# Performance work log

Hardware: AMD Instinct MI355X
Metric: run time of the kernel (lower is better)

The kernel has to match this reference:

```python
import jax, jax.numpy as jnp
import numpy as np

N_PER_TYPE = 32000
N = 3 * N_PER_TYPE          # 96000 nodes
E = N * 16                  # 1,536,000 edges
H, D = 4, 8                 # num_heads, out_dim per head; hidden = 32
IN_DIMS = [128, 64, 32]
NEG_SLOPE = 0.2


def setup_inputs() -> dict:
    key = jax.random.key(0)
    ks = jax.random.split(key, 16)
    inp = {}
    # per-type raw features
    inp['x0'] = jax.random.normal(ks[0], (N_PER_TYPE, IN_DIMS[0]), jnp.float32)
    inp['x1'] = jax.random.normal(ks[1], (N_PER_TYPE, IN_DIMS[1]), jnp.float32)
    inp['x2'] = jax.random.normal(ks[2], (N_PER_TYPE, IN_DIMS[2]), jnp.float32)
    # per-type linear params (fc_list), scaled like kaiming-ish init
    inp['W0'] = jax.random.normal(ks[3], (IN_DIMS[0], H * D), jnp.float32) / np.sqrt(IN_DIMS[0])
    inp['b0'] = jnp.zeros((H * D,), jnp.float32)
    inp['W1'] = jax.random.normal(ks[4], (IN_DIMS[1], H * D), jnp.float32) / np.sqrt(IN_DIMS[1])
    inp['b1'] = jnp.zeros((H * D,), jnp.float32)
    inp['W2'] = jax.random.normal(ks[5], (IN_DIMS[2], H * D), jnp.float32) / np.sqrt(IN_DIMS[2])
    inp['b2'] = jnp.zeros((H * D,), jnp.float32)
    # GAT attention vectors a_l, a_r per head
    inp['attn_l'] = jax.random.normal(ks[6], (H, D), jnp.float32) / np.sqrt(D)
    inp['attn_r'] = jax.random.normal(ks[7], (H, D), jnp.float32) / np.sqrt(D)
    # node types laid out in contiguous blocks -> fixed-size index sets
    inp['type_mask'] = jnp.repeat(jnp.arange(3, dtype=jnp.int32), N_PER_TYPE)
    inp['idx0'] = jnp.arange(0, N_PER_TYPE, dtype=jnp.int32)
    inp['idx1'] = jnp.arange(N_PER_TYPE, 2 * N_PER_TYPE, dtype=jnp.int32)
    inp['idx2'] = jnp.arange(2 * N_PER_TYPE, 3 * N_PER_TYPE, dtype=jnp.int32)
    # random edge list
    inp['src'] = jax.random.randint(ks[8], (E,), 0, N, jnp.int32)
    inp['dst'] = jax.random.randint(ks[9], (E,), 0, N, jnp.int32)
    return inp


def reference(x0, x1, x2, W0, b0, W1, b1, W2, b2, attn_l, attn_r,
              idx0, idx1, idx2, src, dst, type_mask):
    # ---- type-masked per-type linear embed scattered into dense buffer ----
    t = jnp.zeros((N, H * D), x0.dtype)
    t = t.at[idx0].set(x0 @ W0 + b0)
    t = t.at[idx1].set(x1 @ W1 + b1)
    t = t.at[idx2].set(x2 @ W2 + b2)
    # (feat_drop is identity in eval mode)
    h = t.reshape(N, H, D)
    # ---- multi-head GAT attention ----
    el = jnp.einsum('nhd,hd->nh', h, attn_l)   # [N,H]
    er = jnp.einsum('nhd,hd->nh', h, attn_r)   # [N,H]
    e = jax.nn.leaky_relu(el[src] + er[dst], NEG_SLOPE)  # [E,H]
    # segment softmax over incoming edges of each dst node
    m = jax.ops.segment_max(e, dst, num_segments=N)      # [N,H]
    m = jnp.where(jnp.isfinite(m), m, 0.0)               # guard isolated nodes
    ex = jnp.exp(e - m[dst])                             # [E,H]
    s = jax.ops.segment_sum(ex, dst, num_segments=N)     # [N,H]
    alpha = ex / (s[dst] + 1e-9)                         # [E,H]
    # message aggregation
    msg = alpha[:, :, None] * h[src]                     # [E,H,D]
    out = jax.ops.segment_sum(msg, dst, num_segments=N)  # [N,H,D]
    # concat heads + ELU (standard intermediate-layer GAT activation)
    return jax.nn.elu(out).reshape(N, H * D)
```

## Files before the change

kernel.cpp:

```cpp
#include <hip/hip_runtime.h>
#include <hip/hip_bf16.h>
#include <math.h>

#define N_PER_TYPE 32000
#define NN (3 * N_PER_TYPE)
#define EDGES (NN * 16)
#define NHEAD 4
#define HD 32
#define NEG 0.2f
#define BINS 256
#define NPB (NN / BINS)
#define TILES 512
#define TPE (EDGES / TILES)
#define SEG 32
#define MAXBIN 8192
#define EB 375
#define QCH ((TILES * SEG) / 1024)

typedef __attribute__((ext_vector_type(8))) short bf16x8;
typedef __attribute__((ext_vector_type(4))) float f32x4;

__device__ __forceinline__ unsigned packbf(float a, float b) {
    __hip_bfloat162 t = __float22bfloat162_rn(make_float2(a, b));
    return *reinterpret_cast<unsigned*>(&t);
}

__global__ __launch_bounds__(1024) void fused1_kernel(
    const float* __restrict__ x0, const float* __restrict__ x1, const float* __restrict__ x2,
    const float* __restrict__ W0, const float* __restrict__ b0,
    const float* __restrict__ W1, const float* __restrict__ b1,
    const float* __restrict__ W2, const float* __restrict__ b2,
    const float* __restrict__ attn_l, const float* __restrict__ attn_r,
    const int* __restrict__ src, const int* __restrict__ dst,
    __hip_bfloat16* __restrict__ h16, float* __restrict__ el, float* __restrict__ er,
    unsigned* __restrict__ rec2, int* __restrict__ cntT)
{
    __shared__ __align__(16) char smem[43008];
    int blk = blockIdx.x;
    int tid = threadIdx.x;

    if (blk < TILES) {
        int* hist = (int*)smem;
        int* pref = (int*)(smem + 1024);
        unsigned* sorted = (unsigned*)(smem + 2048);
        unsigned char* binof = (unsigned char*)(smem + 2048 + TPE * 4);
        int tile = blk;

        for (int i = tid; i < BINS; i += 1024) hist[i] = 0;
        __syncthreads();

        int e0 = tile * TPE;
        unsigned rv[3]; int rb[3], rk[3]; int ne = 0;
        for (int t = e0 + tid; t < e0 + TPE; t += 1024) {
            int d = dst[t];
            int bin = d / NPB;
            rv[ne] = ((unsigned)src[t] << 9) | (unsigned)(d - bin * NPB);
            rb[ne] = bin;
            rk[ne] = atomicAdd(&hist[bin], 1);
            ++ne;
        }
        __syncthreads();

        if (tid < BINS) pref[tid] = hist[tid];
        __syncthreads();
        #pragma unroll
        for (int off = 1; off < BINS; off <<= 1) {
            int tv = 0;
            if (tid < BINS && tid >= off) tv = pref[tid - off];
            __syncthreads();
            if (tid < BINS) pref[tid] += tv;
            __syncthreads();
        }
        if (tid < BINS) pref[tid] -= hist[tid];
        __syncthreads();

        #pragma unroll
        for (int q = 0; q < 3; ++q) if (q < ne) {
            int p = pref[rb[q]] + rk[q];
            sorted[p] = rv[q];
            binof[p] = (unsigned char)rb[q];
        }
        __syncthreads();

        if (tid < BINS) {
            int c = hist[tid];
            cntT[tile * BINS + tid] = (c > SEG) ? SEG : c;
        }
        for (int j = tid; j < TPE; j += 1024) {
            int bin = binof[j];
            int i = j - pref[bin];
            if (i < SEG)
                rec2[((size_t)bin * TILES + tile) * SEG + i] = sorted[j];
        }
        return;
    }

    unsigned* Wb = (unsigned*)smem;
    float* hepi = (float*)(smem + 8192);

    int eblk = blk - TILES;
    int type = eblk / 125;
    int tb = eblk % 125;

    const float* x; const float* W; const float* bia; int in_dim;
    if (type == 0)      { x = x0; W = W0; bia = b0; in_dim = 128; }
    else if (type == 1) { x = x1; W = W1; bia = b1; in_dim = 64; }
    else                { x = x2; W = W2; bia = b2; in_dim = 32; }
    int KS = in_dim >> 5;

    int ndw = KS << 9;
    for (int i = tid; i < ndw; i += 1024) {
        int d = i & 3, l = (i >> 2) & 63, sn = i >> 8;
        int s = sn >> 1, n = sn & 1;
        int k = (s << 5) + ((l >> 4) << 3) + (d << 1);
        int col = (n << 4) + (l & 15);
        Wb[i] = packbf(W[k * 32 + col], W[(k + 1) * 32 + col]);
    }
    __syncthreads();

    int u = tid >> 8;
    int uwave = (tid >> 6) & 3;
    int lane = tid & 63;
    int node_l0 = u * 64 + uwave * 16 + (lane & 15);
    const float* xrow = x + (size_t)(tb * 256 + node_l0) * in_dim;
    int kg = lane >> 4;

    f32x4 acc0 = {0.f, 0.f, 0.f, 0.f};
    f32x4 acc1 = {0.f, 0.f, 0.f, 0.f};

    for (int s = 0; s < KS; ++s) {
        int k0 = (s << 5) + (kg << 3);
        float4 xa = *(const float4*)(xrow + k0);
        float4 xb = *(const float4*)(xrow + k0 + 4);
        union { unsigned uu[4]; bf16x8 v; } a;
        a.uu[0] = packbf(xa.x, xa.y);
        a.uu[1] = packbf(xa.z, xa.w);
        a.uu[2] = packbf(xb.x, xb.y);
        a.uu[3] = packbf(xb.z, xb.w);
        bf16x8 bfr0 = *(const bf16x8*)&Wb[((s * 2 + 0) * 64 + lane) * 4];
        bf16x8 bfr1 = *(const bf16x8*)&Wb[((s * 2 + 1) * 64 + lane) * 4];
        acc0 = __builtin_amdgcn_mfma_f32_16x16x32_bf16(a.v, bfr0, acc0, 0, 0, 0);
        acc1 = __builtin_amdgcn_mfma_f32_16x16x32_bf16(a.v, bfr1, acc1, 0, 0, 0);
    }

    int hrow = u * 64 + uwave * 16 + ((lane >> 4) << 2);
    int hcol = lane & 15;
    #pragma unroll
    for (int r = 0; r < 4; ++r) {
        hepi[(hrow + r) * 33 + hcol]      = acc0[r];
        hepi[(hrow + r) * 33 + hcol + 16] = acc1[r];
    }
    __syncthreads();

    int node_e = tid >> 2, head = tid & 3;
    int node = type * N_PER_TYPE + tb * 256 + node_e;
    float4 al = *(const float4*)(attn_l + head * 8);
    float4 al2 = *(const float4*)(attn_l + head * 8 + 4);
    float4 ar = *(const float4*)(attn_r + head * 8);
    float4 ar2 = *(const float4*)(attn_r + head * 8 + 4);
    float hv[8];
    #pragma unroll
    for (int i = 0; i < 8; ++i) hv[i] = hepi[node_e * 33 + head * 8 + i] + bia[head * 8 + i];

    float elv = hv[0]*al.x + hv[1]*al.y + hv[2]*al.z + hv[3]*al.w
              + hv[4]*al2.x + hv[5]*al2.y + hv[6]*al2.z + hv[7]*al2.w;
    float erv = hv[0]*ar.x + hv[1]*ar.y + hv[2]*ar.z + hv[3]*ar.w
              + hv[4]*ar2.x + hv[5]*ar2.y + hv[6]*ar2.z + hv[7]*ar2.w;
    el[node * NHEAD + head] = elv;
    er[node * NHEAD + head] = erv;

    uint4 o;
    o.x = packbf(hv[0], hv[1]);
    o.y = packbf(hv[2], hv[3]);
    o.z = packbf(hv[4], hv[5]);
    o.w = packbf(hv[6], hv[7]);
    *reinterpret_cast<uint4*>((unsigned short*)h16 + (size_t)node * HD + head * 8) = o;
}

__global__ __launch_bounds__(1024) void placeagg_kernel(
    const unsigned* __restrict__ rec2, const int* __restrict__ cntT,
    const float* __restrict__ el, const float* __restrict__ er,
    const __hip_bfloat16* __restrict__ h16, float* __restrict__ out)
{
    __shared__ int cnt_l[TILES];
    __shared__ int ncnt[NPB];
    __shared__ int noff[NPB];
    __shared__ int sc[512];
    __shared__ int ldscsr[MAXBIN];

    int k = blockIdx.x, tid = threadIdx.x;
    size_t base = (size_t)k * TILES * SEG;

    for (int i = tid; i < TILES; i += 1024) cnt_l[i] = cntT[i * BINS + k];
    for (int i = tid; i < NPB; i += 1024) ncnt[i] = 0;
    __syncthreads();

    unsigned rv[QCH]; unsigned char rk8[QCH];
    #pragma unroll
    for (int q = 0; q < QCH; ++q) {
        int flat = q * 1024 + tid;
        int t = flat >> 5, i = flat & 31;
        rv[q] = 0xffffffffu;
        if (i < cnt_l[t]) {
            unsigned r = rec2[base + flat];
            rv[q] = r;
            rk8[q] = (unsigned char)atomicAdd(&ncnt[r & 511u], 1);
        }
    }
    __syncthreads();

    int v = 0;
    if (tid < 512) { v = (tid < NPB) ? ncnt[tid] : 0; sc[tid] = v; }
    __syncthreads();
    #pragma unroll
    for (int off = 1; off < 512; off <<= 1) {
        int tv = 0;
        if (tid < 512 && tid >= off) tv = sc[tid - off];
        __syncthreads();
        if (tid < 512) sc[tid] += tv;
        __syncthreads();
    }
    if (tid < NPB) noff[tid] = sc[tid] - v;
    __syncthreads();

    #pragma unroll
    for (int q = 0; q < QCH; ++q) {
        unsigned r = rv[q];
        if (r != 0xffffffffu)
            ldscsr[noff[r & 511u] + (int)rk8[q]] = (int)(r >> 9);
    }
    __syncthreads();

    const unsigned* hp = (const unsigned*)h16;
    int grp = tid >> 4;
    int j = tid & 15;
    int head = j >> 2;
    int hh = j & 3;
    int se0 = j >> 2;

    #pragma unroll
    for (int rnd = 0; rnd < 6; ++rnd) {
        int dl = rnd * 64 + grp;
        if (dl < NPB) {
            int s0 = noff[dl];
            int len = ncnt[dl];
            int node = k * NPB + dl;
            float er_s = er[node * NHEAD + hh];
            float acc0 = 0.f, acc1 = 0.f, den = 0.f;

            for (int bbase = 0; bbase < len; bbase += 16) {
                int rem = len - bbase;
                int svl = (j < rem) ? ldscsr[s0 + bbase + j] : 0;

                float elv[4];
                #pragma unroll
                for (int c4 = 0; c4 < 4; ++c4) {
                    int sv_s = __shfl(svl, (c4 << 2) + se0, 16);
                    elv[c4] = el[sv_s * NHEAD + hh];
                }
                unsigned pw[16];
                #pragma unroll
                for (int c4 = 0; c4 < 4; ++c4) {
                    #pragma unroll
                    for (int i = 0; i < 4; ++i) {
                        int sv = __shfl(svl, (c4 << 2) + i, 16);
                        pw[(c4 << 2) + i] = hp[sv * 16 + j];
                    }
                }
                float exf[4];
                #pragma unroll
                for (int c4 = 0; c4 < 4; ++c4) {
                    float xs = elv[c4] + er_s;
                    xs = fmaxf(xs, NEG * xs);
                    int se = (c4 << 2) + se0;
                    exf[c4] = (se < rem) ? __expf(xs) : 0.0f;
                }
                #pragma unroll
                for (int c4 = 0; c4 < 4; ++c4) {
                    #pragma unroll
                    for (int i = 0; i < 4; ++i) {
                        float ex = __shfl(exf[c4], (i << 2) + head, 16);
                        unsigned p = pw[(c4 << 2) + i];
                        den += ex;
                        acc0 = fmaf(ex, __uint_as_float(p << 16),         acc0);
                        acc1 = fmaf(ex, __uint_as_float(p & 0xffff0000u), acc1);
                    }
                }
            }
            den += 1e-9f;
            float v0 = acc0 / den, v1 = acc1 / den;
            v0 = v0 > 0.f ? v0 : expm1f(v0);
            v1 = v1 > 0.f ? v1 : expm1f(v1);
            *reinterpret_cast<float2*>(out + node * HD + (j << 1)) = make_float2(v0, v1);
        }
    }
}

extern "C" void kernel_launch(void* const* d_in, const int* in_sizes, int n_in,
                              void* d_out, int out_size, void* d_ws, size_t ws_size,
                              hipStream_t stream) {
    const float* x0 = (const float*)d_in[0];
    const float* x1 = (const float*)d_in[1];
    const float* x2 = (const float*)d_in[2];
    const float* W0 = (const float*)d_in[3];
    const float* b0 = (const float*)d_in[4];
    const float* W1 = (const float*)d_in[5];
    const float* b1 = (const float*)d_in[6];
    const float* W2 = (const float*)d_in[7];
    const float* b2 = (const float*)d_in[8];
    const float* attn_l = (const float*)d_in[9];
    const float* attn_r = (const float*)d_in[10];
    const int* src = (const int*)d_in[15];
    const int* dst = (const int*)d_in[16];
    float* out = (float*)d_out;

    __hip_bfloat16* h16 = (__hip_bfloat16*)d_ws;
    float* el = (float*)(h16 + NN * HD);
    float* er = el + NN * NHEAD;
    int* cntT = (int*)(er + NN * NHEAD);
    unsigned* rec2 = (unsigned*)(cntT + TILES * BINS);

    fused1_kernel<<<TILES + EB, 1024, 0, stream>>>(
        x0, x1, x2, W0, b0, W1, b1, W2, b2, attn_l, attn_r,
        src, dst, h16, el, er, rec2, cntT);
    placeagg_kernel<<<BINS, 1024, 0, stream>>>(rec2, cntT, el, er, h16, out);
}
```

Measured before the change: 58.92 us.

## Split bf16 features into head-pair halves and aggregate in two passes

```diff
diff --git a/kernel.cpp b/kernel.cpp
--- a/kernel.cpp
+++ b/kernel.cpp
@@ -32,7 +32,8 @@
     const float* __restrict__ W2, const float* __restrict__ b2,
     const float* __restrict__ attn_l, const float* __restrict__ attn_r,
     const int* __restrict__ src, const int* __restrict__ dst,
-    __hip_bfloat16* __restrict__ h16, float* __restrict__ el, float* __restrict__ er,
+    unsigned short* __restrict__ h_lo, unsigned short* __restrict__ h_hi,
+    float* __restrict__ el, float* __restrict__ er,
     unsigned* __restrict__ rec2, int* __restrict__ cntT)
 {
     __shared__ __align__(16) char smem[43008];
@@ -90,7 +91,8 @@
             int bin = binof[j];
             int i = j - pref[bin];
             if (i < SEG)
-                rec2[((size_t)bin * TILES + tile) * SEG + i] = sorted[j];
+                __builtin_nontemporal_store(sorted[j],
+                    &rec2[((size_t)bin * TILES + tile) * SEG + i]);
         }
         return;
     }
@@ -174,13 +176,15 @@
     o.y = packbf(hv[2], hv[3]);
     o.z = packbf(hv[4], hv[5]);
     o.w = packbf(hv[6], hv[7]);
-    *reinterpret_cast<uint4*>((unsigned short*)h16 + (size_t)node * HD + head * 8) = o;
+    unsigned short* hdst = (head < 2) ? h_lo : h_hi;
+    *reinterpret_cast<uint4*>(hdst + (size_t)node * 16 + (head & 1) * 8) = o;
 }
 
 __global__ __launch_bounds__(1024) void placeagg_kernel(
     const unsigned* __restrict__ rec2, const int* __restrict__ cntT,
     const float* __restrict__ el, const float* __restrict__ er,
-    const __hip_bfloat16* __restrict__ h16, float* __restrict__ out)
+    const unsigned short* __restrict__ h_lo, const unsigned short* __restrict__ h_hi,
+    float* __restrict__ out)
 {
     __shared__ int cnt_l[TILES];
     __shared__ int ncnt[NPB];
@@ -202,7 +206,7 @@
         int t = flat >> 5, i = flat & 31;
         rv[q] = 0xffffffffu;
         if (i < cnt_l[t]) {
-            unsigned r = rec2[base + flat];
+            unsigned r = __builtin_nontemporal_load(&rec2[base + flat]);
             rv[q] = r;
             rk8[q] = (unsigned char)atomicAdd(&ncnt[r & 511u], 1);
         }
@@ -231,67 +235,55 @@
     }
     __syncthreads();
 
-    const unsigned* hp = (const unsigned*)h16;
     int grp = tid >> 4;
     int j = tid & 15;
-    int head = j >> 2;
-    int hh = j & 3;
-    int se0 = j >> 2;
-
-    #pragma unroll
-    for (int rnd = 0; rnd < 6; ++rnd) {
-        int dl = rnd * 64 + grp;
-        if (dl < NPB) {
-            int s0 = noff[dl];
-            int len = ncnt[dl];
-            int node = k * NPB + dl;
-            float er_s = er[node * NHEAD + hh];
-            float acc0 = 0.f, acc1 = 0.f, den = 0.f;
-
-            for (int bbase = 0; bbase < len; bbase += 16) {
-                int rem = len - bbase;
-                int svl = (j < rem) ? ldscsr[s0 + bbase + j] : 0;
-
-                float elv[4];
-                #pragma unroll
-                for (int c4 = 0; c4 < 4; ++c4) {
-                    int sv_s = __shfl(svl, (c4 << 2) + se0, 16);
-                    elv[c4] = el[sv_s * NHEAD + hh];
-                }
-                unsigned pw[16];
-                #pragma unroll
-                for (int c4 = 0; c4 < 4; ++c4) {
+    bool hiHead = (j >= 8);
+
+    #pragma unroll
+    for (int hf = 0; hf < 2; ++hf) {
+        const unsigned short* hp = hf ? h_hi : h_lo;
+        int hh0 = hf * 2;
+
+        #pragma unroll
+        for (int rnd = 0; rnd < 6; ++rnd) {
+            int dl = rnd * 64 + grp;
+            if (dl < NPB) {
+                int s0 = noff[dl];
+                int len = ncnt[dl];
+                int node = k * NPB + dl;
+                float2 er2 = *(const float2*)(er + node * NHEAD + hh0);
+                float acc = 0.f, den = 0.f;
+
+                for (int bbase = 0; bbase < len; bbase += 16) {
+                    int rem = len - bbase;
+                    int svl = (j < rem) ? ldscsr[s0 + bbase + j] : 0;
+
+                    float2 elp = *(const float2*)(el + svl * NHEAD + hh0);
+                    float x0 = elp.x + er2.x; x0 = fmaxf(x0, NEG * x0);
+                    float x1 = elp.y + er2.y; x1 = fmaxf(x1, NEG * x1);
+                    float e0 = (j < rem) ? __expf(x0) : 0.0f;
+                    float e1 = (j < rem) ? __expf(x1) : 0.0f;
+
+                    unsigned short pw[16];
                     #pragma unroll
-                    for (int i = 0; i < 4; ++i) {
-                        int sv = __shfl(svl, (c4 << 2) + i, 16);
-                        pw[(c4 << 2) + i] = hp[sv * 16 + j];
+                    for (int e = 0; e < 16; ++e) {
+                        int sv = __shfl(svl, e, 16);
+                        pw[e] = hp[(size_t)sv * 16 + j];
+                    }
+                    #pragma unroll
+                    for (int e = 0; e < 16; ++e) {
+                        float ex0 = __shfl(e0, e, 16);
+                        float ex1 = __shfl(e1, e, 16);
+                        float ex = hiHead ? ex1 : ex0;
+                        den += ex;
+                        acc = fmaf(ex, __uint_as_float(((unsigned)pw[e]) << 16), acc);
                     }
                 }
-                float exf[4];
-                #pragma unroll
-                for (int c4 = 0; c4 < 4; ++c4) {
-                    float xs = elv[c4] + er_s;
-                    xs = fmaxf(xs, NEG * xs);
-                    int se = (c4 << 2) + se0;
-                    exf[c4] = (se < rem) ? __expf(xs) : 0.0f;
-                }
-                #pragma unroll
-                for (int c4 = 0; c4 < 4; ++c4) {
-                    #pragma unroll
-                    for (int i = 0; i < 4; ++i) {
-                        float ex = __shfl(exf[c4], (i << 2) + head, 16);
-                        unsigned p = pw[(c4 << 2) + i];
-                        den += ex;
-                        acc0 = fmaf(ex, __uint_as_float(p << 16),         acc0);
-                        acc1 = fmaf(ex, __uint_as_float(p & 0xffff0000u), acc1);
-                    }
-                }
+                den += 1e-9f;
+                float vo = acc / den;
+                vo = vo > 0.f ? vo : expm1f(vo);
+                __builtin_nontemporal_store(vo, &out[node * HD + hf * 16 + j]);
             }
-            den += 1e-9f;
-            float v0 = acc0 / den, v1 = acc1 / den;
-            v0 = v0 > 0.f ? v0 : expm1f(v0);
-            v1 = v1 > 0.f ? v1 : expm1f(v1);
-            *reinterpret_cast<float2*>(out + node * HD + (j << 1)) = make_float2(v0, v1);
         }
     }
 }
@@ -314,14 +306,15 @@
     const int* dst = (const int*)d_in[16];
     float* out = (float*)d_out;
 
-    __hip_bfloat16* h16 = (__hip_bfloat16*)d_ws;
-    float* el = (float*)(h16 + NN * HD);
+    unsigned short* h_lo = (unsigned short*)d_ws;
+    unsigned short* h_hi = h_lo + (size_t)NN * 16;
+    float* el = (float*)(h_hi + (size_t)NN * 16);
     float* er = el + NN * NHEAD;
     int* cntT = (int*)(er + NN * NHEAD);
     unsigned* rec2 = (unsigned*)(cntT + TILES * BINS);
 
     fused1_kernel<<<TILES + EB, 1024, 0, stream>>>(
         x0, x1, x2, W0, b0, W1, b1, W2, b2, attn_l, attn_r,
-        src, dst, h16, el, er, rec2, cntT);
-    placeagg_kernel<<<BINS, 1024, 0, stream>>>(rec2, cntT, el, er, h16, out);
+        src, dst, h_lo, h_hi, el, er, rec2, cntT);
+    placeagg_kernel<<<BINS, 1024, 0, stream>>>(rec2, cntT, el, er, h_lo, h_hi, out);
 }
```

After: 89.40 us. 51.7% more time.
